# Performance work log

Hardware: AMD Instinct MI355X
Metric: run time of the kernel (lower is better)

Reference implementation:

```python
import jax, jax.numpy as jnp
import numpy as np

NUM_QUBITS = 21
NUM_LAYERS = 4
ACTION_DIM = 18
STATE_DIM = 2 ** NUM_QUBITS  # amplitude register size


def _rx(t):
    c = jnp.cos(t / 2)
    s = jnp.sin(t / 2)
    return jnp.stack([jnp.stack([c + 0j, -1j * s]), jnp.stack([-1j * s, c + 0j])]).astype(jnp.complex64)


def _ry(t):
    c = jnp.cos(t / 2)
    s = jnp.sin(t / 2)
    return jnp.stack([jnp.stack([c, -s]), jnp.stack([s, c])]).astype(jnp.complex64)


def _rz(t):
    e = jnp.exp(-1j * t / 2).astype(jnp.complex64)
    z = jnp.zeros_like(e)
    return jnp.stack([jnp.stack([e, z]), jnp.stack([z, jnp.conj(e)])])


def apply_1q(psi, U, q):
    # wire 0 is the most-significant bit (PennyLane convention)
    s = psi.reshape(2 ** q, 2, -1)
    s = jnp.einsum('ab,xbz->xaz', U, s)
    return s.reshape(-1)


def apply_cnot(psi, c, t):
    a, b = (c, t) if c < t else (t, c)
    s = psi.reshape(2 ** a, 2, 2 ** (b - a - 1), 2, -1)
    ctrl_ax = 1 if c < t else 3
    tgt_ax = 3 if c < t else 1
    s0 = jax.lax.index_in_dim(s, 0, axis=ctrl_ax, keepdims=False)
    s1 = jax.lax.index_in_dim(s, 1, axis=ctrl_ax, keepdims=False)
    tgt_in_slab = tgt_ax if tgt_ax < ctrl_ax else tgt_ax - 1
    s1 = jnp.flip(s1, axis=tgt_in_slab)  # X on target where control==1
    s = jnp.stack([s0, s1], axis=ctrl_ax)
    return s.reshape(-1)


def _layer(psi, lp, entangle):
    # lp: (NUM_QUBITS, 3) rotation angles for this layer
    for q in range(NUM_QUBITS):
        psi = apply_1q(psi, _rx(lp[q, 0]), q)
        psi = apply_1q(psi, _ry(lp[q, 1]), q)
        psi = apply_1q(psi, _rz(lp[q, 2]), q)
    if entangle:
        for q in range(NUM_QUBITS - 1):
            psi = apply_cnot(psi, q, q + 1)
        psi = apply_cnot(psi, NUM_QUBITS - 1, 0)
    return psi


def setup_inputs() -> dict:
    key = jax.random.key(0)
    k1, k2, k3, k4 = jax.random.split(key, 4)
    state = jax.random.normal(k1, (STATE_DIM,), dtype=jnp.float32)
    circuit_params = jax.random.normal(k2, (NUM_LAYERS * NUM_QUBITS * 3,), dtype=jnp.float32) * 0.01
    bound = 1.0 / np.sqrt(NUM_QUBITS)
    head_w = jax.random.uniform(k3, (ACTION_DIM, NUM_QUBITS), jnp.float32, -bound, bound)
    head_b = jax.random.uniform(k4, (ACTION_DIM,), jnp.float32, -bound, bound)
    return {'state': state, 'circuit_params': circuit_params, 'head_w': head_w, 'head_b': head_b}


def reference(state, circuit_params, head_w, head_b):
    # Amplitude encoding: normalize (state_dim == 2**num_qubits so no padding needed)
    norm = jnp.linalg.norm(state)
    inv = jnp.where(norm > 0, 1.0 / jnp.maximum(norm, 1e-30), 0.0)
    basis0 = jnp.zeros((STATE_DIM,), jnp.float32).at[0].set(1.0)
    amp = jnp.where(norm > 0, state * inv, basis0)
    psi = amp.astype(jnp.complex64)

    lp = circuit_params.reshape(NUM_LAYERS, NUM_QUBITS, 3)
    for layer in range(NUM_LAYERS):
        psi = _layer(psi, lp[layer], layer < NUM_LAYERS - 1)

    # Pauli-Z expectation values per qubit from |psi|^2
    probs = psi.real ** 2 + psi.imag ** 2
    zvals = []
    for q in range(NUM_QUBITS):
        p = probs.reshape(2 ** q, 2, -1)
        zvals.append(p[:, 0, :].sum() - p[:, 1, :].sum())
    meas = jnp.stack(zvals).astype(jnp.float32)

    logits = head_w @ meas + head_b
    return jax.nn.softmax(logits, axis=-1)
```

## Files before the change

kernel.cpp:

```cpp
#include <hip/hip_runtime.h>

#define NQ 21
#define DIM (1 << NQ)
#define NL 4
#define ADIM 18
#define GB 512
#define NT 512

__device__ __forceinline__ float2 cfma2(float2 u0, float2 a, float2 u1, float2 b) {
    return make_float2(u0.x * a.x - u0.y * a.y + u1.x * b.x - u1.y * b.y,
                       u0.x * a.y + u0.y * a.x + u1.x * b.y + u1.y * b.x);
}

struct GateU { float2 u00, u01, u10, u11; };

__device__ __forceinline__ void bfly(float2& a, float2& b, const GateU& U) {
    float2 na = cfma2(U.u00, a, U.u01, b);
    float2 nb = cfma2(U.u10, a, U.u11, b);
    a = na; b = nb;
}

__device__ __forceinline__ int sw(int j) { return j ^ (((j >> 4) & 7) << 1); }

__device__ __forceinline__ void make_mats(GateU* mats, const float* __restrict__ cp, int layer, int tid) {
    if (tid < NQ) {
        const float* ang = cp + (layer * NQ + tid) * 3;
        float a = ang[0], b = ang[1], c = ang[2];
        float ca = cosf(0.5f * a), sa = sinf(0.5f * a);
        float cb = cosf(0.5f * b), sb = sinf(0.5f * b);
        float cc = cosf(0.5f * c), sc = sinf(0.5f * c);
        float2 m00 = make_float2(cb * ca,  sb * sa);
        float2 m01 = make_float2(-sb * ca, -cb * sa);
        float2 m10 = make_float2(sb * ca,  -cb * sa);
        float2 m11 = make_float2(cb * ca,  -sb * sa);
        GateU U;
        U.u00 = make_float2(cc * m00.x + sc * m00.y, cc * m00.y - sc * m00.x);
        U.u01 = make_float2(cc * m01.x + sc * m01.y, cc * m01.y - sc * m01.x);
        U.u10 = make_float2(cc * m10.x - sc * m10.y, cc * m10.y + sc * m10.x);
        U.u11 = make_float2(cc * m11.x - sc * m11.y, cc * m11.y + sc * m11.x);
        mats[tid] = U;
    }
}

__global__ __launch_bounds__(NT, 4) void k_passB(const float* __restrict__ state,
                                                 float2* __restrict__ psi,
                                                 const float* __restrict__ cp, int layer) {
    __shared__ float2 tile[4096];
    __shared__ GateU mats[NQ];
    const int tid = threadIdx.x;
    const int blk = (blockIdx.x & 7) * 64 + (blockIdx.x >> 3);
    float4* psi4 = (float4*)psi;
    float4* t4 = (float4*)tile;

    if (layer == 0) {
        const float4* s4 = (const float4*)state;
        for (int it = 0; it < 2; ++it) {
            int f2 = it * NT + tid;
            int h = f2 >> 1, c2 = f2 & 1;
            float4 w = s4[(h << 10) | (blk << 1) | c2];
            int j = 8 * h + 4 * c2;
            t4[sw(j) >> 1]     = make_float4(w.x, 0.f, w.y, 0.f);
            t4[sw(j + 2) >> 1] = make_float4(w.z, 0.f, w.w, 0.f);
        }
        make_mats(mats, cp, layer, tid);
        __syncthreads();
        for (int kb = 0; kb <= 8; ++kb) {
            GateU U = mats[8 - kb];
            for (int it = 0; it < 4; ++it) {
                int p = it * NT + tid;
                int l = p & 7, hp = p >> 3;
                int h0 = ((hp >> kb) << (kb + 1)) | (hp & ((1 << kb) - 1));
                int i0 = h0 * 8 + l;
                bfly(tile[sw(i0)], tile[sw(i0 + (8 << kb))], U);
            }
            __syncthreads();
        }
    } else {
        float2 v[8];
        float4 w[4];
        for (int i = 0; i < 4; ++i) {
            int f = i * NT + tid;
            int h = f >> 2, c = f & 3;
            w[i] = psi4[(h << 11) | (blk << 2) | c];
        }
        make_mats(mats, cp, layer, tid);
        __syncthreads();
#pragma unroll
        for (int i = 0; i < 4; ++i) {
            v[2 * i]     = make_float2(w[i].x, w[i].y);
            v[2 * i + 1] = make_float2(w[i ^ 2].z, w[i ^ 2].w);
        }
        GateU U0 = mats[0];
#pragma unroll
        for (int s = 0; s < 8; ++s) if (!(s & 4)) bfly(v[s], v[s | 4], U0);
        GateU U1 = mats[1];
#pragma unroll
        for (int s = 0; s < 8; ++s) if (!(s & 2)) bfly(v[s], v[s | 2], U1);
        for (int i = 0; i < 4; ++i)
            t4[sw(2 * (i * NT + tid)) >> 1] =
                make_float4(v[2 * i].x, v[2 * i].y, v[2 * i + 1].x, v[2 * i + 1].y);
        __syncthreads();
        for (int kb = 0; kb <= 6; ++kb) {
            GateU U = mats[8 - kb];
            for (int it = 0; it < 4; ++it) {
                int p = it * NT + tid;
                int l = p & 7, hp = p >> 3;
                int h0 = ((hp >> kb) << (kb + 1)) | (hp & ((1 << kb) - 1));
                int i0 = h0 * 8 + l;
                bfly(tile[sw(i0)], tile[sw(i0 + (8 << kb))], U);
            }
            __syncthreads();
        }
    }
    int srcmask = (layer < 3) ? 0xFF : 0;
    for (int i = 0; i < 4; ++i) {
        int f = i * NT + tid;
        int h = f >> 2, c = f & 3;
        int hs = h ^ ((h >> 1) & srcmask);
        int j = sw(hs * 8 + 2 * c);
        float2 e0 = tile[j], e1 = tile[j + 1];
        psi4[(h << 11) | (blk << 2) | c] = make_float4(e0.x, e0.y, e1.x, e1.y);
    }
}

__global__ __launch_bounds__(NT, 4) void k_passA(float2* __restrict__ psi,
                                                 const float* __restrict__ cp, int layer,
                                                 float* __restrict__ partials) {
    __shared__ float2 tile[4096];
    __shared__ GateU mats[NQ];
    const int tid = threadIdx.x, blk = blockIdx.x;
    float4* psi4 = (float4*)psi;
    float4* t4 = (float4*)tile;

    {
        const float4* ga = psi4 + (size_t)blk * 2048;
        float2 v[8];
        float4 w[4];
        for (int i = 0; i < 4; ++i) w[i] = ga[i * NT + tid];
        make_mats(mats, cp, layer, tid);
        __syncthreads();
#pragma unroll
        for (int i = 0; i < 4; ++i) {
            v[2 * i]     = make_float2(w[i].x, w[i].y);
            v[2 * i + 1] = make_float2(w[i].z, w[i].w);
        }
        GateU U20 = mats[20];
#pragma unroll
        for (int s = 0; s < 8; s += 2) bfly(v[s], v[s + 1], U20);
        GateU U10 = mats[10];
#pragma unroll
        for (int s = 0; s < 8; ++s) if (!(s & 2)) bfly(v[s], v[s | 2], U10);
        GateU U9 = mats[9];
#pragma unroll
        for (int s = 0; s < 8; ++s) if (!(s & 4)) bfly(v[s], v[s | 4], U9);
        for (int i = 0; i < 4; ++i)
            t4[sw(2 * (i * NT + tid)) >> 1] =
                make_float4(v[2 * i].x, v[2 * i].y, v[2 * i + 1].x, v[2 * i + 1].y);
    }
    __syncthreads();
    for (int k = 1; k <= 9; ++k) {
        GateU U = mats[20 - k];
        int m = 1 << k;
        for (int it = 0; it < 4; ++it) {
            int p = it * NT + tid;
            int i0 = ((p >> k) << (k + 1)) | (p & (m - 1));
            bfly(tile[sw(i0)], tile[sw(i0 | m)], U);
        }
        __syncthreads();
    }
    if (layer < 3) {
        float4* oa = psi4 + (size_t)blk * 2048;
        int cb = (blk & 1) << 11;
        for (int i = 0; i < 4; ++i) {
            int f = i * NT + tid;
            int s0 = ((2 * f) ^ (f & 0x7FF)) ^ cb;
            float2 e0 = tile[sw(s0)], e1 = tile[sw(s0 ^ 1)];
            oa[f] = make_float4(e0.x, e0.y, e1.x, e1.y);
        }
    } else {
        float tot = 0.f, ones[NQ];
#pragma unroll
        for (int q = 0; q < NQ; ++q) ones[q] = 0.f;
        for (int it = 0; it < 8; ++it) {
            int j = it * NT + tid;
            float2 a2 = tile[sw(j)];
            float pr = a2.x * a2.x + a2.y * a2.y;
            int gidx = (blk << 12) | j;
            tot += pr;
#pragma unroll
            for (int q = 0; q < NQ; ++q)
                ones[q] += pr * (float)((gidx >> (20 - q)) & 1);
        }
        for (int off = 32; off; off >>= 1) {
            tot += __shfl_down(tot, off, 64);
#pragma unroll
            for (int q = 0; q < NQ; ++q) ones[q] += __shfl_down(ones[q], off, 64);
        }
        __syncthreads();
        float* red = (float*)tile;
        int wv = tid >> 6, ln = tid & 63;
        if (ln == 0) {
            red[wv * 22 + 21] = tot;
#pragma unroll
            for (int q = 0; q < NQ; ++q) red[wv * 22 + q] = ones[q];
        }
        __syncthreads();
        if (tid < 22) {
            float s = 0.f;
            for (int wvi = 0; wvi < 8; ++wvi) s += red[wvi * 22 + tid];
            partials[blk * 22 + tid] = s;
        }
    }
}

__global__ __launch_bounds__(NT) void k_final(const float* __restrict__ partials,
                                              const float* __restrict__ head_w,
                                              const float* __restrict__ head_b,
                                              float* __restrict__ out) {
    __shared__ float red[640];
    __shared__ float meas[NQ];
    __shared__ float lg[ADIM];
    int tid = threadIdx.x;
    int col = tid % 22, grp = tid / 22;
    if (tid < 506) {
        float s = 0.f;
        for (int r = grp; r < GB; r += 23) s += partials[r * 22 + col];
        red[grp * 22 + col] = s;
    }
    __syncthreads();
    if (tid < 22) {
        float t2 = 0.f;
        for (int g = 0; g < 23; ++g) t2 += red[g * 22 + tid];
        red[600 + tid] = t2;
    }
    __syncthreads();
    if (tid < NQ) {
        float tot = red[600 + 21];
        meas[tid] = (tot > 0.f) ? (1.f - 2.f * red[600 + tid] / tot) : 1.f;
    }
    __syncthreads();
    if (tid < ADIM) {
        float s2 = head_b[tid];
        for (int q = 0; q < NQ; ++q) s2 += head_w[tid * NQ + q] * meas[q];
        lg[tid] = s2;
    }
    __syncthreads();
    if (tid == 0) {
        float m = lg[0];
        for (int a = 1; a < ADIM; ++a) m = fmaxf(m, lg[a]);
        float ssum = 0.f;
        for (int a = 0; a < ADIM; ++a) ssum += expf(lg[a] - m);
        float inv = 1.f / ssum;
        for (int a = 0; a < ADIM; ++a) out[a] = expf(lg[a] - m) * inv;
    }
}

extern "C" void kernel_launch(void* const* d_in, const int* in_sizes, int n_in,
                              void* d_out, int out_size, void* d_ws, size_t ws_size,
                              hipStream_t stream) {
    const float* state   = (const float*)d_in[0];
    const float* cparams = (const float*)d_in[1];
    const float* head_w  = (const float*)d_in[2];
    const float* head_b  = (const float*)d_in[3];
    float* out = (float*)d_out;

    float2* psi      = (float2*)d_ws;
    float*  partials = (float*)((char*)d_ws + (size_t)DIM * 8);

    for (int layer = 0; layer < NL; ++layer) {
        k_passB<<<GB, NT, 0, stream>>>(state, psi, cparams, layer);
        k_passA<<<GB, NT, 0, stream>>>(psi, cparams, layer, partials);
    }
    k_final<<<1, NT, 0, stream>>>(partials, head_w, head_b, out);
}
```

Before: 227.3 us.

## Fuse three qubit butterflies per shared-memory round in register radix-8 passes

Replaces the per-qubit shared-memory butterfly loops with a round3 helper. Each thread loads 8 amplitudes spanning three adjacent qubit bits, applies three gates in registers, and writes them back. This cuts shared-memory traffic and the number of __syncthreads barriers to roughly a third. It also removes the blockIdx swizzle in k_passB, which changes the global-memory access order across blocks and risks worse DRAM/cache locality.

New measurement: 207.9 us. -8.5%, faster.

```diff
diff --git a/kernel.cpp b/kernel.cpp
--- a/kernel.cpp
+++ b/kernel.cpp
@@ -42,13 +42,30 @@
     }
 }
 
+__device__ __forceinline__ void round3(float2* tile, int tid, int g,
+                                       GateU Ua, GateU Ub, GateU Uc) {
+    int bl = (1 << g) - 1;
+    int base = (tid & bl) | ((tid >> g) << (g + 3));
+    float2 v[8];
+#pragma unroll
+    for (int j = 0; j < 8; ++j) v[j] = tile[sw(base + (j << g))];
+#pragma unroll
+    for (int s = 0; s < 8; s += 2) bfly(v[s], v[s + 1], Ua);
+#pragma unroll
+    for (int s = 0; s < 8; ++s) if (!(s & 2)) bfly(v[s], v[s | 2], Ub);
+#pragma unroll
+    for (int s = 0; s < 8; ++s) if (!(s & 4)) bfly(v[s], v[s | 4], Uc);
+#pragma unroll
+    for (int j = 0; j < 8; ++j) tile[sw(base + (j << g))] = v[j];
+    __syncthreads();
+}
+
 __global__ __launch_bounds__(NT, 4) void k_passB(const float* __restrict__ state,
                                                  float2* __restrict__ psi,
                                                  const float* __restrict__ cp, int layer) {
     __shared__ float2 tile[4096];
     __shared__ GateU mats[NQ];
-    const int tid = threadIdx.x;
-    const int blk = (blockIdx.x & 7) * 64 + (blockIdx.x >> 3);
+    const int tid = threadIdx.x, blk = blockIdx.x;
     float4* psi4 = (float4*)psi;
     float4* t4 = (float4*)tile;
 
@@ -64,17 +81,9 @@
         }
         make_mats(mats, cp, layer, tid);
         __syncthreads();
-        for (int kb = 0; kb <= 8; ++kb) {
-            GateU U = mats[8 - kb];
-            for (int it = 0; it < 4; ++it) {
-                int p = it * NT + tid;
-                int l = p & 7, hp = p >> 3;
-                int h0 = ((hp >> kb) << (kb + 1)) | (hp & ((1 << kb) - 1));
-                int i0 = h0 * 8 + l;
-                bfly(tile[sw(i0)], tile[sw(i0 + (8 << kb))], U);
-            }
-            __syncthreads();
-        }
+        round3(tile, tid, 3, mats[8], mats[7], mats[6]);
+        round3(tile, tid, 6, mats[5], mats[4], mats[3]);
+        round3(tile, tid, 9, mats[2], mats[1], mats[0]);
     } else {
         float2 v[8];
         float4 w[4];
@@ -100,14 +109,14 @@
             t4[sw(2 * (i * NT + tid)) >> 1] =
                 make_float4(v[2 * i].x, v[2 * i].y, v[2 * i + 1].x, v[2 * i + 1].y);
         __syncthreads();
-        for (int kb = 0; kb <= 6; ++kb) {
-            GateU U = mats[8 - kb];
+        round3(tile, tid, 3, mats[8], mats[7], mats[6]);
+        round3(tile, tid, 6, mats[5], mats[4], mats[3]);
+        {
+            GateU U = mats[2];
             for (int it = 0; it < 4; ++it) {
                 int p = it * NT + tid;
-                int l = p & 7, hp = p >> 3;
-                int h0 = ((hp >> kb) << (kb + 1)) | (hp & ((1 << kb) - 1));
-                int i0 = h0 * 8 + l;
-                bfly(tile[sw(i0)], tile[sw(i0 + (8 << kb))], U);
+                int i0 = ((p >> 9) << 10) | (p & 511);
+                bfly(tile[sw(i0)], tile[sw(i0 | 512)], U);
             }
             __syncthreads();
         }
@@ -158,16 +167,10 @@
                 make_float4(v[2 * i].x, v[2 * i].y, v[2 * i + 1].x, v[2 * i + 1].y);
     }
     __syncthreads();
-    for (int k = 1; k <= 9; ++k) {
-        GateU U = mats[20 - k];
-        int m = 1 << k;
-        for (int it = 0; it < 4; ++it) {
-            int p = it * NT + tid;
-            int i0 = ((p >> k) << (k + 1)) | (p & (m - 1));
-            bfly(tile[sw(i0)], tile[sw(i0 | m)], U);
-        }
-        __syncthreads();
-    }
+    round3(tile, tid, 1, mats[19], mats[18], mats[17]);
+    round3(tile, tid, 4, mats[16], mats[15], mats[14]);
+    round3(tile, tid, 7, mats[13], mats[12], mats[11]);
+
     if (layer < 3) {
         float4* oa = psi4 + (size_t)blk * 2048;
         int cb = (blk & 1) << 11;
```
